# Optimization experiments

Hardware: AMD Instinct MI355X
Metric: run time of the kernel (lower is better)

## Reference

```python
import jax, jax.numpy as jnp
import numpy as np

N, E = 50000, 800000
IN, HID, OUT, T = 96, 128, 64, 8
THETA = 0.5


def setup_inputs() -> dict:
    key = jax.random.key(0)
    ks = jax.random.split(key, 8)
    x = jax.random.normal(ks[0], (N, IN), dtype=jnp.float32)
    edge_weight = jax.random.uniform(ks[1], (E,), dtype=jnp.float32)
    W1 = jax.random.normal(ks[2], (IN, HID), dtype=jnp.float32) * (2.0 / np.sqrt(IN + HID))
    W2 = jax.random.normal(ks[3], (HID, OUT), dtype=jnp.float32) * (2.0 / np.sqrt(HID + OUT))
    # Bernoulli(1 - theta) masks, fixed per MC sample (created in __init__)
    mask1 = (jax.random.uniform(ks[4], (T, IN, HID)) < (1.0 - THETA)).astype(jnp.float32)
    mask2 = (jax.random.uniform(ks[5], (T, HID, OUT)) < (1.0 - THETA)).astype(jnp.float32)
    src = jax.random.randint(ks[6], (E,), 0, N, dtype=jnp.int32)
    dst = jax.random.randint(ks[7], (E,), 0, N, dtype=jnp.int32)
    return {"x": x, "edge_weight": edge_weight, "W1": W1, "W2": W2,
            "mask1": mask1, "mask2": mask2, "src": src, "dst": dst}


def _spmm(feat, edge_weight, src, dst, n_nodes):
    # u_mul_e('feat','edge_weight') followed by fn.sum onto dst nodes
    msg = feat[src] * edge_weight[:, None]          # [E, D]
    return jax.ops.segment_sum(msg, dst, num_segments=n_nodes)  # [N, D]


def reference(x, edge_weight, W1, W2, mask1, mask2, src, dst):
    n = x.shape[0]
    # first aggregation is mask-independent -> compute once, share across T samples
    agg1 = _spmm(x, edge_weight, src, dst, n)       # [N, IN]

    def per_sample(m1, m2):
        h = jax.nn.relu(agg1 @ (W1 * m1))           # [N, HID]
        agg2 = _spmm(h, edge_weight, src, dst, n)   # [N, HID]
        return agg2 @ (W2 * m2)                     # [N, OUT]

    # stack of the T per-sample outputs (torch version returns a list)
    return jax.vmap(per_sample)(mask1, mask2)       # [T, N, OUT]
```

## Files before the change

kernel.cpp:

```cpp
#include <hip/hip_runtime.h>

#define N_NODES 50000
#define N_EDGES 800000
#define IN_F 96
#define HID_F 128
#define OUT_F 64
#define T_S 8
#define SCAN_B 196

typedef __attribute__((ext_vector_type(8))) short short8;
typedef __attribute__((ext_vector_type(4))) float float4v;
typedef __attribute__((ext_vector_type(2))) unsigned uint2v;
typedef __attribute__((ext_vector_type(4))) unsigned uint4v;

__device__ __forceinline__ float bf2f(unsigned short h) {
    unsigned u = ((unsigned)h) << 16;
    float f;
    __builtin_memcpy(&f, &u, 4);
    return f;
}
__device__ __forceinline__ unsigned short f2bf(float f) {
    unsigned u;
    __builtin_memcpy(&u, &f, 4);
    unsigned r = (u + 0x7fffu + ((u >> 16) & 1u)) >> 16;
    return (unsigned short)r;
}
__device__ __forceinline__ float bf_lo(unsigned u) {
    unsigned v = u << 16;
    float f;
    __builtin_memcpy(&f, &v, 4);
    return f;
}
__device__ __forceinline__ float bf_hi(unsigned u) {
    unsigned v = u & 0xffff0000u;
    float f;
    __builtin_memcpy(&f, &v, 4);
    return f;
}

__global__ void k_count(const int* __restrict__ dst, int* __restrict__ cnt) {
    int e = blockIdx.x * 256 + threadIdx.x;
    if (e < N_EDGES) atomicAdd(&cnt[dst[e]], 1);
}

__global__ __launch_bounds__(256) void k_scan1(const int* __restrict__ cnt,
                                               int* __restrict__ excl,
                                               int* __restrict__ blockSums) {
    __shared__ int buf[256];
    int tid = threadIdx.x;
    int idx = blockIdx.x * 256 + tid;
    int v = (idx < N_NODES) ? cnt[idx] : 0;
    buf[tid] = v;
    __syncthreads();
    for (int off = 1; off < 256; off <<= 1) {
        int t = buf[tid];
        int u = (tid >= off) ? buf[tid - off] : 0;
        __syncthreads();
        buf[tid] = t + u;
        __syncthreads();
    }
    int incl = buf[tid];
    if (idx < N_NODES) excl[idx] = incl - v;
    if (tid == 255) blockSums[blockIdx.x] = incl;
}

__global__ __launch_bounds__(256) void k_scan2(const int* __restrict__ blockSums,
                                               int* __restrict__ blockOff) {
    __shared__ int buf[256];
    int tid = threadIdx.x;
    int v = (tid < SCAN_B) ? blockSums[tid] : 0;
    buf[tid] = v;
    __syncthreads();
    for (int off = 1; off < 256; off <<= 1) {
        int t = buf[tid];
        int u = (tid >= off) ? buf[tid - off] : 0;
        __syncthreads();
        buf[tid] = t + u;
        __syncthreads();
    }
    if (tid < SCAN_B) blockOff[tid] = buf[tid] - v;
}

__global__ __launch_bounds__(256) void k_scan3(const int* __restrict__ excl,
                                               const int* __restrict__ blockOff,
                                               int* __restrict__ row_ptr,
                                               int* __restrict__ cursor) {
    int idx = blockIdx.x * 256 + threadIdx.x;
    if (idx < N_NODES) {
        int p = excl[idx] + blockOff[blockIdx.x];
        row_ptr[idx] = p;
        cursor[idx] = p;
    }
    if (idx == 0) row_ptr[N_NODES] = N_EDGES;
}

__global__ void k_fill(const int* __restrict__ src, const int* __restrict__ dst,
                       const float* __restrict__ ew, int* __restrict__ cursor,
                       uint2v* __restrict__ csr) {
    int e = blockIdx.x * 256 + threadIdx.x;
    if (e < N_EDGES) {
        int d = dst[e];
        int pos = atomicAdd(&cursor[d], 1);
        uint2v c;
        c.x = (unsigned)src[e];
        c.y = __float_as_uint(ew[e]);
        __builtin_nontemporal_store(c, &csr[pos]);
    }
}

__global__ void k_xb(const float* __restrict__ x, unsigned short* __restrict__ xb) {
    int i = blockIdx.x * 256 + threadIdx.x;
    int idx = i * 4;
    if (idx < N_NODES * IN_F) {
        float4v v = __builtin_nontemporal_load((const float4v*)(x + idx));
        uint2v r;
        r.x = (unsigned)f2bf(v.x) | ((unsigned)f2bf(v.y) << 16);
        r.y = (unsigned)f2bf(v.z) | ((unsigned)f2bf(v.w) << 16);
        *(uint2v*)(xb + idx) = r;
    }
}

__global__ __launch_bounds__(256) void k_spmm1(const unsigned short* __restrict__ xb,
                                               const int* __restrict__ row_ptr,
                                               const uint2v* __restrict__ csr,
                                               unsigned short* __restrict__ agg1) {
    int wave = threadIdx.x >> 6, lane = threadIdx.x & 63;
    int node = blockIdx.x * 4 + wave;
    if (lane >= 48) return;
    int beg = row_ptr[node], end = row_ptr[node + 1];
    const unsigned* xrow = (const unsigned*)xb;
    float a0 = 0.f, a1 = 0.f;
    int e = beg;
    for (; e + 7 < end; e += 8) {
        uint2v c[8];
        unsigned d[8];
#pragma unroll
        for (int i = 0; i < 8; i++) c[i] = __builtin_nontemporal_load(&csr[e + i]);
#pragma unroll
        for (int i = 0; i < 8; i++) d[i] = xrow[(size_t)c[i].x * 48 + lane];
#pragma unroll
        for (int i = 0; i < 8; i++) {
            float wv = __uint_as_float(c[i].y);
            a0 = fmaf(wv, bf_lo(d[i]), a0);
            a1 = fmaf(wv, bf_hi(d[i]), a1);
        }
    }
    for (; e + 3 < end; e += 4) {
        uint2v c[4];
        unsigned d[4];
#pragma unroll
        for (int i = 0; i < 4; i++) c[i] = __builtin_nontemporal_load(&csr[e + i]);
#pragma unroll
        for (int i = 0; i < 4; i++) d[i] = xrow[(size_t)c[i].x * 48 + lane];
#pragma unroll
        for (int i = 0; i < 4; i++) {
            float wv = __uint_as_float(c[i].y);
            a0 = fmaf(wv, bf_lo(d[i]), a0);
            a1 = fmaf(wv, bf_hi(d[i]), a1);
        }
    }
    for (; e < end; e++) {
        uint2v c = __builtin_nontemporal_load(&csr[e]);
        float wv = __uint_as_float(c.y);
        unsigned d = xrow[(size_t)c.x * 48 + lane];
        a0 = fmaf(wv, bf_lo(d), a0);
        a1 = fmaf(wv, bf_hi(d), a1);
    }
    unsigned pk = (unsigned)f2bf(a0) | ((unsigned)f2bf(a1) << 16);
    __builtin_nontemporal_store(pk, (unsigned*)agg1 + (size_t)node * 48 + lane);
}

__global__ void k_wprep(const float* __restrict__ W1, const float* __restrict__ W2,
                        const float* __restrict__ m1, const float* __restrict__ m2,
                        unsigned short* __restrict__ wf) {
    int gid = blockIdx.x * 256 + threadIdx.x;
    if (gid >= T_S * 20480) return;
    int t = gid / 20480;
    int idx = gid % 20480;
    float val;
    if (idx < 12288) {
        int j = idx & 7, lane = (idx >> 3) & 63, fr = idx >> 9;
        int kk = fr >> 3, nt = fr & 7;
        int k = kk * 32 + (lane >> 4) * 8 + j;
        int n = nt * 16 + (lane & 15);
        val = W1[k * HID_F + n] * m1[((size_t)t * IN_F + k) * HID_F + n];
    } else {
        int i2 = idx - 12288;
        int j = i2 & 7, lane = (i2 >> 3) & 63, fr = i2 >> 9;
        int kk = fr >> 2, ot = fr & 3;
        int k = kk * 32 + (lane >> 4) * 8 + j;
        int o = ot * 16 + (lane & 15);
        val = W2[k * OUT_F + o] * m2[((size_t)t * HID_F + k) * OUT_F + o];
    }
    wf[gid] = f2bf(val);
}

__global__ __launch_bounds__(256) void k_gemm(const unsigned short* __restrict__ agg1,
                                              const unsigned short* __restrict__ wfrags,
                                              unsigned short* __restrict__ P, int tBase,
                                              int nodeStride, int tMul) {
    __shared__ __align__(16) unsigned short ldsW[20480];
    __shared__ __align__(16) unsigned short ldsH[4][2176];
    int t = tBase + blockIdx.y;
    const uint4* wsrc = (const uint4*)(wfrags + (size_t)t * 20480);
    uint4* wdst = (uint4*)ldsW;
    for (int i = threadIdx.x; i < 2560; i += 256) wdst[i] = wsrc[i];
    __syncthreads();

    int wave = threadIdx.x >> 6, lane = threadIdx.x & 63;
    int quad = lane >> 4, l15 = lane & 15;

    for (int it = 0; it < 4; it++) {
        int node = blockIdx.x * 256 + it * 64 + wave * 16 + l15;
        bool v = node < N_NODES;

        short8 a[3];
        if (v) {
            const unsigned short* ap = agg1 + (size_t)node * IN_F;
            a[0] = *(const short8*)(ap + 0 * 32 + quad * 8);
            a[1] = *(const short8*)(ap + 1 * 32 + quad * 8);
            a[2] = *(const short8*)(ap + 2 * 32 + quad * 8);
        } else {
            short8 z = {0, 0, 0, 0, 0, 0, 0, 0};
            a[0] = z; a[1] = z; a[2] = z;
        }

        for (int nt = 0; nt < 8; nt++) {
            float4v acc = {0.f, 0.f, 0.f, 0.f};
            for (int kk = 0; kk < 3; kk++) {
                short8 w = *(const short8*)&ldsW[(kk * 8 + nt) * 512 + lane * 8];
                acc = __builtin_amdgcn_mfma_f32_16x16x32_bf16(w, a[kk], acc, 0, 0, 0);
            }
            unsigned h0 = f2bf(fmaxf(acc[0], 0.f));
            unsigned h1 = f2bf(fmaxf(acc[1], 0.f));
            unsigned h2 = f2bf(fmaxf(acc[2], 0.f));
            unsigned h3 = f2bf(fmaxf(acc[3], 0.f));
            uint2 pk;
            pk.x = h0 | (h1 << 16);
            pk.y = h2 | (h3 << 16);
            *(uint2*)&ldsH[wave][l15 * 136 + nt * 16 + quad * 4] = pk;
        }

        short8 hf[4];
        for (int kk = 0; kk < 4; kk++)
            hf[kk] = *(const short8*)&ldsH[wave][l15 * 136 + kk * 32 + quad * 8];

        unsigned short* Pt = P + (size_t)node * nodeStride + (size_t)t * tMul;
        for (int ot = 0; ot < 4; ot++) {
            float4v acc = {0.f, 0.f, 0.f, 0.f};
            for (int kk = 0; kk < 4; kk++) {
                short8 w = *(const short8*)&ldsW[12288 + (kk * 4 + ot) * 512 + lane * 8];
                acc = __builtin_amdgcn_mfma_f32_16x16x32_bf16(w, hf[kk], acc, 0, 0, 0);
            }
            if (v) {
                uint2v pk;
                pk.x = (unsigned)f2bf(acc[0]) | ((unsigned)f2bf(acc[1]) << 16);
                pk.y = (unsigned)f2bf(acc[2]) | ((unsigned)f2bf(acc[3]) << 16);
                __builtin_nontemporal_store(pk, (uint2v*)(Pt + ot * 16 + quad * 4));
            }
        }
    }
}

__global__ __launch_bounds__(256) void k_spmm2(const unsigned short* __restrict__ P,
                                               const int* __restrict__ row_ptr,
                                               const uint2v* __restrict__ csr,
                                               float* __restrict__ out) {
    int wave = threadIdx.x >> 6, lane = threadIdx.x & 63;
    int node = blockIdx.x * 4 + wave;
    int beg = row_ptr[node], end = row_ptr[node + 1];
    const uint4v* Pl = (const uint4v*)P + lane;
    float acc[8] = {0.f, 0.f, 0.f, 0.f, 0.f, 0.f, 0.f, 0.f};
    int e = beg;
    for (; e + 7 < end; e += 8) {
        uint2v c[8];
        uint4v d[8];
#pragma unroll
        for (int i = 0; i < 8; i++) c[i] = __builtin_nontemporal_load(&csr[e + i]);
#pragma unroll
        for (int i = 0; i < 8; i++) d[i] = Pl[(size_t)c[i].x * 64];
#pragma unroll
        for (int i = 0; i < 8; i++) {
            float wv = __uint_as_float(c[i].y);
            acc[0] = fmaf(wv, bf_lo(d[i].x), acc[0]);
            acc[1] = fmaf(wv, bf_hi(d[i].x), acc[1]);
            acc[2] = fmaf(wv, bf_lo(d[i].y), acc[2]);
            acc[3] = fmaf(wv, bf_hi(d[i].y), acc[3]);
            acc[4] = fmaf(wv, bf_lo(d[i].z), acc[4]);
            acc[5] = fmaf(wv, bf_hi(d[i].z), acc[5]);
            acc[6] = fmaf(wv, bf_lo(d[i].w), acc[6]);
            acc[7] = fmaf(wv, bf_hi(d[i].w), acc[7]);
        }
    }
    for (; e + 3 < end; e += 4) {
        uint2v c[4];
        uint4v d[4];
#pragma unroll
        for (int i = 0; i < 4; i++) c[i] = __builtin_nontemporal_load(&csr[e + i]);
#pragma unroll
        for (int i = 0; i < 4; i++) d[i] = Pl[(size_t)c[i].x * 64];
#pragma unroll
        for (int i = 0; i < 4; i++) {
            float wv = __uint_as_float(c[i].y);
            acc[0] = fmaf(wv, bf_lo(d[i].x), acc[0]);
            acc[1] = fmaf(wv, bf_hi(d[i].x), acc[1]);
            acc[2] = fmaf(wv, bf_lo(d[i].y), acc[2]);
            acc[3] = fmaf(wv, bf_hi(d[i].y), acc[3]);
            acc[4] = fmaf(wv, bf_lo(d[i].z), acc[4]);
            acc[5] = fmaf(wv, bf_hi(d[i].z), acc[5]);
            acc[6] = fmaf(wv, bf_lo(d[i].w), acc[6]);
            acc[7] = fmaf(wv, bf_hi(d[i].w), acc[7]);
        }
    }
    for (; e < end; e++) {
        uint2v c = __builtin_nontemporal_load(&csr[e]);
        float wv = __uint_as_float(c.y);
        uint4v d = Pl[(size_t)c.x * 64];
        acc[0] = fmaf(wv, bf_lo(d.x), acc[0]);
        acc[1] = fmaf(wv, bf_hi(d.x), acc[1]);
        acc[2] = fmaf(wv, bf_lo(d.y), acc[2]);
        acc[3] = fmaf(wv, bf_hi(d.y), acc[3]);
        acc[4] = fmaf(wv, bf_lo(d.z), acc[4]);
        acc[5] = fmaf(wv, bf_hi(d.z), acc[5]);
        acc[6] = fmaf(wv, bf_lo(d.w), acc[6]);
        acc[7] = fmaf(wv, bf_hi(d.w), acc[7]);
    }
    int t = lane >> 3, o = (lane & 7) * 8;
    float* op = out + ((size_t)t * N_NODES + node) * OUT_F + o;
    float4v v0 = {acc[0], acc[1], acc[2], acc[3]};
    float4v v1 = {acc[4], acc[5], acc[6], acc[7]};
    __builtin_nontemporal_store(v0, (float4v*)op);
    __builtin_nontemporal_store(v1, (float4v*)(op + 4));
}

__global__ __launch_bounds__(512) void k_spmm2_1t(const unsigned short* __restrict__ P,
                                                  const int* __restrict__ row_ptr,
                                                  const uint2v* __restrict__ csr,
                                                  float* __restrict__ out) {
    int node = blockIdx.x * 8 + (threadIdx.x >> 6);
    int o = threadIdx.x & 63;
    if (node >= N_NODES) return;
    int beg = row_ptr[node], end = row_ptr[node + 1];
    const unsigned short* Pt = P + o;
    float a0 = 0.f, a1 = 0.f, a2 = 0.f, a3 = 0.f;
    int e = beg;
    for (; e + 3 < end; e += 4) {
        uint2v c0 = __builtin_nontemporal_load(&csr[e]);
        uint2v c1 = __builtin_nontemporal_load(&csr[e + 1]);
        uint2v c2 = __builtin_nontemporal_load(&csr[e + 2]);
        uint2v c3 = __builtin_nontemporal_load(&csr[e + 3]);
        a0 += __uint_as_float(c0.y) * bf2f(Pt[(size_t)c0.x * OUT_F]);
        a1 += __uint_as_float(c1.y) * bf2f(Pt[(size_t)c1.x * OUT_F]);
        a2 += __uint_as_float(c2.y) * bf2f(Pt[(size_t)c2.x * OUT_F]);
        a3 += __uint_as_float(c3.y) * bf2f(Pt[(size_t)c3.x * OUT_F]);
    }
    for (; e < end; e++) {
        uint2v c = __builtin_nontemporal_load(&csr[e]);
        a0 += __uint_as_float(c.y) * bf2f(Pt[(size_t)c.x * OUT_F]);
    }
    out[(size_t)node * OUT_F + o] = a0 + a1 + a2 + a3;
}

extern "C" void kernel_launch(void* const* d_in, const int* in_sizes, int n_in,
                              void* d_out, int out_size, void* d_ws, size_t ws_size,
                              hipStream_t stream) {
    const float* x = (const float*)d_in[0];
    const float* ew = (const float*)d_in[1];
    const float* W1 = (const float*)d_in[2];
    const float* W2 = (const float*)d_in[3];
    const float* m1 = (const float*)d_in[4];
    const float* m2 = (const float*)d_in[5];
    const int* src = (const int*)d_in[6];
    const int* dst = (const int*)d_in[7];
    float* out = (float*)d_out;

    char* w = (char*)d_ws;
    size_t off = 0;
    auto alloc = [&](size_t bytes) -> void* {
        void* p = (void*)(w + off);
        off += (bytes + 255) & ~(size_t)255;
        return p;
    };
    int* cnt = (int*)alloc((size_t)N_NODES * 4);
    int* row_ptr = (int*)alloc((size_t)(N_NODES + 1) * 4);
    int* cursor = (int*)alloc((size_t)N_NODES * 4);
    int* excl = (int*)alloc((size_t)N_NODES * 4);
    int* blockSums = (int*)alloc((size_t)SCAN_B * 4);
    int* blockOff = (int*)alloc((size_t)SCAN_B * 4);
    uint2v* csr = (uint2v*)alloc((size_t)N_EDGES * 8);
    unsigned short* agg1 = (unsigned short*)alloc((size_t)N_NODES * IN_F * 2);
    unsigned short* wf = (unsigned short*)alloc((size_t)T_S * 20480 * 2);

    size_t unionBase = off;
    size_t pBytesBatched = (size_t)T_S * N_NODES * OUT_F * 2;
    size_t xbBytes = (size_t)N_NODES * IN_F * 2;
    bool batched = ws_size >= unionBase + (pBytesBatched > xbBytes ? pBytesBatched : xbBytes);
    unsigned short* xb = (unsigned short*)(w + unionBase);
    unsigned short* P = (unsigned short*)(w + unionBase);
    if (!batched) {
        xb = (unsigned short*)(w + unionBase);
        P = (unsigned short*)(w + unionBase + ((xbBytes + 255) & ~(size_t)255));
    }

    hipMemsetAsync(cnt, 0, (size_t)N_NODES * 4, stream);
    k_count<<<N_EDGES / 256, 256, 0, stream>>>(dst, cnt);
    k_scan1<<<SCAN_B, 256, 0, stream>>>(cnt, excl, blockSums);
    k_scan2<<<1, 256, 0, stream>>>(blockSums, blockOff);
    k_scan3<<<SCAN_B, 256, 0, stream>>>(excl, blockOff, row_ptr, cursor);
    k_fill<<<N_EDGES / 256, 256, 0, stream>>>(src, dst, ew, cursor, csr);
    k_xb<<<(N_NODES * IN_F / 4 + 255) / 256, 256, 0, stream>>>(x, xb);
    k_spmm1<<<N_NODES / 4, 256, 0, stream>>>(xb, row_ptr, csr, agg1);
    k_wprep<<<(T_S * 20480) / 256, 256, 0, stream>>>(W1, W2, m1, m2, wf);

    if (batched) {
        k_gemm<<<dim3(196, 8), 256, 0, stream>>>(agg1, wf, P, 0, T_S * OUT_F, OUT_F);
        k_spmm2<<<N_NODES / 4, 256, 0, stream>>>(P, row_ptr, csr, out);
    } else {
        for (int t = 0; t < T_S; t++) {
            k_gemm<<<dim3(196, 1), 256, 0, stream>>>(agg1, wf, P, t, OUT_F, 0);
            k_spmm2_1t<<<6250, 512, 0, stream>>>(P, row_ptr, csr,
                                                 out + (size_t)t * N_NODES * OUT_F);
        }
    }
}
```

Measured before the change: 423.9 us.

## Merge setup kernels, collapse scan stages, drop nontemporal hints, enlarge GEMM tiles

Fuses the edge-count, x-to-bf16 conversion and weight/mask prep into one launch, and folds the block-offset scan into the final scan kernel, cutting the number of kernel launches. Nontemporal loads and stores on the CSR, agg1, P and output buffers become ordinary accesses so these reused arrays can stay in cache. The GEMM now handles 512 nodes per block over 8 iterations with half the grid, adding a barrier between iterations. Risks are lower GEMM parallelism and extra cache pressure from the normal stores.

```diff
diff --git a/kernel.cpp b/kernel.cpp
--- a/kernel.cpp
+++ b/kernel.cpp
@@ -8,6 +8,11 @@
 #define T_S 8
 #define SCAN_B 196
 
+#define NB_COUNT 3125
+#define NB_XB 4688
+#define NB_WPREP 640
+#define NB_INIT (NB_COUNT + NB_XB + NB_WPREP)
+
 typedef __attribute__((ext_vector_type(8))) short short8;
 typedef __attribute__((ext_vector_type(4))) float float4v;
 typedef __attribute__((ext_vector_type(2))) unsigned uint2v;
@@ -38,12 +43,60 @@
     return f;
 }
 
-__global__ void k_count(const int* __restrict__ dst, int* __restrict__ cnt) {
-    int e = blockIdx.x * 256 + threadIdx.x;
-    if (e < N_EDGES) atomicAdd(&cnt[dst[e]], 1);
-}
-
-__global__ __launch_bounds__(256) void k_scan1(const int* __restrict__ cnt,
+__global__ __launch_bounds__(256) void k_init(const int* __restrict__ dst,
+                                              int* __restrict__ cnt,
+                                              const float* __restrict__ x,
+                                              unsigned short* __restrict__ xb,
+                                              const float* __restrict__ W1,
+                                              const float* __restrict__ W2,
+                                              const float* __restrict__ m1,
+                                              const float* __restrict__ m2,
+                                              unsigned short* __restrict__ wf) {
+    int bid = blockIdx.x;
+    if (bid < NB_COUNT) {
+        int e = bid * 256 + threadIdx.x;
+        if (e < N_EDGES) atomicAdd(&cnt[dst[e]], 1);
+        return;
+    }
+    bid -= NB_COUNT;
+    if (bid < NB_XB) {
+        int i = bid * 256 + threadIdx.x;
+        int idx = i * 4;
+        if (idx < N_NODES * IN_F) {
+            float4v v = __builtin_nontemporal_load((const float4v*)(x + idx));
+            uint2v r;
+            r.x = (unsigned)f2bf(v.x) | ((unsigned)f2bf(v.y) << 16);
+            r.y = (unsigned)f2bf(v.z) | ((unsigned)f2bf(v.w) << 16);
+            *(uint2v*)(xb + idx) = r;
+        }
+        return;
+    }
+    bid -= NB_XB;
+    {
+        int gid = bid * 256 + threadIdx.x;
+        if (gid >= T_S * 20480) return;
+        int t = gid / 20480;
+        int idx = gid % 20480;
+        float val;
+        if (idx < 12288) {
+            int j = idx & 7, lane = (idx >> 3) & 63, fr = idx >> 9;
+            int kk = fr >> 3, nt = fr & 7;
+            int k = kk * 32 + (lane >> 4) * 8 + j;
+            int n = nt * 16 + (lane & 15);
+            val = W1[k * HID_F + n] * m1[((size_t)t * IN_F + k) * HID_F + n];
+        } else {
+            int i2 = idx - 12288;
+            int j = i2 & 7, lane = (i2 >> 3) & 63, fr = i2 >> 9;
+            int kk = fr >> 2, ot = fr & 3;
+            int k = kk * 32 + (lane >> 4) * 8 + j;
+            int o = ot * 16 + (lane & 15);
+            val = W2[k * OUT_F + o] * m2[((size_t)t * HID_F + k) * OUT_F + o];
+        }
+        wf[gid] = f2bf(val);
+    }
+}
+
+__global__ __launch_bounds__(256) void k_scanA(const int* __restrict__ cnt,
                                                int* __restrict__ excl,
                                                int* __restrict__ blockSums) {
     __shared__ int buf[256];
@@ -64,8 +117,10 @@
     if (tid == 255) blockSums[blockIdx.x] = incl;
 }
 
-__global__ __launch_bounds__(256) void k_scan2(const int* __restrict__ blockSums,
-                                               int* __restrict__ blockOff) {
+__global__ __launch_bounds__(256) void k_scanB(const int* __restrict__ excl,
+                                               const int* __restrict__ blockSums,
+                                               int* __restrict__ row_ptr,
+                                               int* __restrict__ cursor) {
     __shared__ int buf[256];
     int tid = threadIdx.x;
     int v = (tid < SCAN_B) ? blockSums[tid] : 0;
@@ -78,16 +133,12 @@
         buf[tid] = t + u;
         __syncthreads();
     }
-    if (tid < SCAN_B) blockOff[tid] = buf[tid] - v;
-}
-
-__global__ __launch_bounds__(256) void k_scan3(const int* __restrict__ excl,
-                                               const int* __restrict__ blockOff,
-                                               int* __restrict__ row_ptr,
-                                               int* __restrict__ cursor) {
-    int idx = blockIdx.x * 256 + threadIdx.x;
+    __shared__ int base;
+    if (tid == 0) base = (blockIdx.x == 0) ? 0 : buf[blockIdx.x - 1];
+    __syncthreads();
+    int idx = blockIdx.x * 256 + tid;
     if (idx < N_NODES) {
-        int p = excl[idx] + blockOff[blockIdx.x];
+        int p = excl[idx] + base;
         row_ptr[idx] = p;
         cursor[idx] = p;
     }
@@ -105,18 +156,6 @@
         c.x = (unsigned)src[e];
         c.y = __float_as_uint(ew[e]);
         __builtin_nontemporal_store(c, &csr[pos]);
-    }
-}
-
-__global__ void k_xb(const float* __restrict__ x, unsigned short* __restrict__ xb) {
-    int i = blockIdx.x * 256 + threadIdx.x;
-    int idx = i * 4;
-    if (idx < N_NODES * IN_F) {
-        float4v v = __builtin_nontemporal_load((const float4v*)(x + idx));
-        uint2v r;
-        r.x = (unsigned)f2bf(v.x) | ((unsigned)f2bf(v.y) << 16);
-        r.y = (unsigned)f2bf(v.z) | ((unsigned)f2bf(v.w) << 16);
-        *(uint2v*)(xb + idx) = r;
     }
 }
 
@@ -135,7 +174,7 @@
         uint2v c[8];
         unsigned d[8];
 #pragma unroll
-        for (int i = 0; i < 8; i++) c[i] = __builtin_nontemporal_load(&csr[e + i]);
+        for (int i = 0; i < 8; i++) c[i] = csr[e + i];
 #pragma unroll
         for (int i = 0; i < 8; i++) d[i] = xrow[(size_t)c[i].x * 48 + lane];
 #pragma unroll
@@ -149,7 +188,7 @@
         uint2v c[4];
         unsigned d[4];
 #pragma unroll
-        for (int i = 0; i < 4; i++) c[i] = __builtin_nontemporal_load(&csr[e + i]);
+        for (int i = 0; i < 4; i++) c[i] = csr[e + i];
 #pragma unroll
         for (int i = 0; i < 4; i++) d[i] = xrow[(size_t)c[i].x * 48 + lane];
 #pragma unroll
@@ -160,39 +199,14 @@
         }
     }
     for (; e < end; e++) {
-        uint2v c = __builtin_nontemporal_load(&csr[e]);
+        uint2v c = csr[e];
         float wv = __uint_as_float(c.y);
         unsigned d = xrow[(size_t)c.x * 48 + lane];
         a0 = fmaf(wv, bf_lo(d), a0);
         a1 = fmaf(wv, bf_hi(d), a1);
     }
-    unsigned pk = (unsigned)f2bf(a0) | ((unsigned)f2bf(a1) << 16);
-    __builtin_nontemporal_store(pk, (unsigned*)agg1 + (size_t)node * 48 + lane);
-}
-
-__global__ void k_wprep(const float* __restrict__ W1, const float* __restrict__ W2,
-                        const float* __restrict__ m1, const float* __restrict__ m2,
-                        unsigned short* __restrict__ wf) {
-    int gid = blockIdx.x * 256 + threadIdx.x;
-    if (gid >= T_S * 20480) return;
-    int t = gid / 20480;
-    int idx = gid % 20480;
-    float val;
-    if (idx < 12288) {
-        int j = idx & 7, lane = (idx >> 3) & 63, fr = idx >> 9;
-        int kk = fr >> 3, nt = fr & 7;
-        int k = kk * 32 + (lane >> 4) * 8 + j;
-        int n = nt * 16 + (lane & 15);
-        val = W1[k * HID_F + n] * m1[((size_t)t * IN_F + k) * HID_F + n];
-    } else {
-        int i2 = idx - 12288;
-        int j = i2 & 7, lane = (i2 >> 3) & 63, fr = i2 >> 9;
-        int kk = fr >> 2, ot = fr & 3;
-        int k = kk * 32 + (lane >> 4) * 8 + j;
-        int o = ot * 16 + (lane & 15);
-        val = W2[k * OUT_F + o] * m2[((size_t)t * HID_F + k) * OUT_F + o];
-    }
-    wf[gid] = f2bf(val);
+    ((unsigned*)agg1)[(size_t)node * 48 + lane] =
+        (unsigned)f2bf(a0) | ((unsigned)f2bf(a1) << 16);
 }
 
 __global__ __launch_bounds__(256) void k_gemm(const unsigned short* __restrict__ agg1,
@@ -210,8 +224,8 @@
     int wave = threadIdx.x >> 6, lane = threadIdx.x & 63;
     int quad = lane >> 4, l15 = lane & 15;
 
-    for (int it = 0; it < 4; it++) {
-        int node = blockIdx.x * 256 + it * 64 + wave * 16 + l15;
+    for (int it = 0; it < 8; it++) {
+        int node = blockIdx.x * 512 + it * 64 + wave * 16 + l15;
         bool v = node < N_NODES;
 
         short8 a[3];
@@ -253,12 +267,13 @@
                 acc = __builtin_amdgcn_mfma_f32_16x16x32_bf16(w, hf[kk], acc, 0, 0, 0);
             }
             if (v) {
-                uint2v pk;
+                uint2 pk;
                 pk.x = (unsigned)f2bf(acc[0]) | ((unsigned)f2bf(acc[1]) << 16);
                 pk.y = (unsigned)f2bf(acc[2]) | ((unsigned)f2bf(acc[3]) << 16);
-                __builtin_nontemporal_store(pk, (uint2v*)(Pt + ot * 16 + quad * 4));
+                *(uint2*)(Pt + ot * 16 + quad * 4) = pk;
             }
         }
+        if (it < 7) __syncthreads();
     }
 }
 
@@ -276,7 +291,7 @@
         uint2v c[8];
         uint4v d[8];
 #pragma unroll
-        for (int i = 0; i < 8; i++) c[i] = __builtin_nontemporal_load(&csr[e + i]);
+        for (int i = 0; i < 8; i++) c[i] = csr[e + i];
 #pragma unroll
         for (int i = 0; i < 8; i++) d[i] = Pl[(size_t)c[i].x * 64];
 #pragma unroll
@@ -296,7 +311,7 @@
         uint2v c[4];
         uint4v d[4];
 #pragma unroll
-        for (int i = 0; i < 4; i++) c[i] = __builtin_nontemporal_load(&csr[e + i]);
+        for (int i = 0; i < 4; i++) c[i] = csr[e + i];
 #pragma unroll
         for (int i = 0; i < 4; i++) d[i] = Pl[(size_t)c[i].x * 64];
 #pragma unroll
@@ -313,7 +328,7 @@
         }
     }
     for (; e < end; e++) {
-        uint2v c = __builtin_nontemporal_load(&csr[e]);
+        uint2v c = csr[e];
         float wv = __uint_as_float(c.y);
         uint4v d = Pl[(size_t)c.x * 64];
         acc[0] = fmaf(wv, bf_lo(d.x), acc[0]);
@@ -329,8 +344,8 @@
     float* op = out + ((size_t)t * N_NODES + node) * OUT_F + o;
     float4v v0 = {acc[0], acc[1], acc[2], acc[3]};
     float4v v1 = {acc[4], acc[5], acc[6], acc[7]};
-    __builtin_nontemporal_store(v0, (float4v*)op);
-    __builtin_nontemporal_store(v1, (float4v*)(op + 4));
+    *(float4v*)op = v0;
+    *(float4v*)(op + 4) = v1;
 }
 
 __global__ __launch_bounds__(512) void k_spmm2_1t(const unsigned short* __restrict__ P,
@@ -345,17 +360,17 @@
     float a0 = 0.f, a1 = 0.f, a2 = 0.f, a3 = 0.f;
     int e = beg;
     for (; e + 3 < end; e += 4) {
-        uint2v c0 = __builtin_nontemporal_load(&csr[e]);
-        uint2v c1 = __builtin_nontemporal_load(&csr[e + 1]);
-        uint2v c2 = __builtin_nontemporal_load(&csr[e + 2]);
-        uint2v c3 = __builtin_nontemporal_load(&csr[e + 3]);
+        uint2v c0 = csr[e];
+        uint2v c1 = csr[e + 1];
+        uint2v c2 = csr[e + 2];
+        uint2v c3 = csr[e + 3];
         a0 += __uint_as_float(c0.y) * bf2f(Pt[(size_t)c0.x * OUT_F]);
         a1 += __uint_as_float(c1.y) * bf2f(Pt[(size_t)c1.x * OUT_F]);
         a2 += __uint_as_float(c2.y) * bf2f(Pt[(size_t)c2.x * OUT_F]);
         a3 += __uint_as_float(c3.y) * bf2f(Pt[(size_t)c3.x * OUT_F]);
     }
     for (; e < end; e++) {
-        uint2v c = __builtin_nontemporal_load(&csr[e]);
+        uint2v c = csr[e];
         a0 += __uint_as_float(c.y) * bf2f(Pt[(size_t)c.x * OUT_F]);
     }
     out[(size_t)node * OUT_F + o] = a0 + a1 + a2 + a3;
@@ -386,7 +401,6 @@
     int* cursor = (int*)alloc((size_t)N_NODES * 4);
     int* excl = (int*)alloc((size_t)N_NODES * 4);
     int* blockSums = (int*)alloc((size_t)SCAN_B * 4);
-    int* blockOff = (int*)alloc((size_t)SCAN_B * 4);
     uint2v* csr = (uint2v*)alloc((size_t)N_EDGES * 8);
     unsigned short* agg1 = (unsigned short*)alloc((size_t)N_NODES * IN_F * 2);
     unsigned short* wf = (unsigned short*)alloc((size_t)T_S * 20480 * 2);
@@ -403,21 +417,18 @@
     }
 
     hipMemsetAsync(cnt, 0, (size_t)N_NODES * 4, stream);
-    k_count<<<N_EDGES / 256, 256, 0, stream>>>(dst, cnt);
-    k_scan1<<<SCAN_B, 256, 0, stream>>>(cnt, excl, blockSums);
-    k_scan2<<<1, 256, 0, stream>>>(blockSums, blockOff);
-    k_scan3<<<SCAN_B, 256, 0, stream>>>(excl, blockOff, row_ptr, cursor);
+    k_init<<<NB_INIT, 256, 0, stream>>>(dst, cnt, x, xb, W1, W2, m1, m2, wf);
+    k_scanA<<<SCAN_B, 256, 0, stream>>>(cnt, excl, blockSums);
+    k_scanB<<<SCAN_B, 256, 0, stream>>>(excl, blockSums, row_ptr, cursor);
     k_fill<<<N_EDGES / 256, 256, 0, stream>>>(src, dst, ew, cursor, csr);
-    k_xb<<<(N_NODES * IN_F / 4 + 255) / 256, 256, 0, stream>>>(x, xb);
     k_spmm1<<<N_NODES / 4, 256, 0, stream>>>(xb, row_ptr, csr, agg1);
-    k_wprep<<<(T_S * 20480) / 256, 256, 0, stream>>>(W1, W2, m1, m2, wf);
 
     if (batched) {
-        k_gemm<<<dim3(196, 8), 256, 0, stream>>>(agg1, wf, P, 0, T_S * OUT_F, OUT_F);
+        k_gemm<<<dim3(98, 8), 256, 0, stream>>>(agg1, wf, P, 0, T_S * OUT_F, OUT_F);
         k_spmm2<<<N_NODES / 4, 256, 0, stream>>>(P, row_ptr, csr, out);
     } else {
         for (int t = 0; t < T_S; t++) {
-            k_gemm<<<dim3(196, 1), 256, 0, stream>>>(agg1, wf, P, t, OUT_F, 0);
+            k_gemm<<<dim3(98, 1), 256, 0, stream>>>(agg1, wf, P, t, OUT_F, 0);
             k_spmm2_1t<<<6250, 512, 0, stream>>>(P, row_ptr, csr,
                                                  out + (size_t)t * N_NODES * OUT_F);
         }
```

Result: faster. 407.0 us (-4.0%).
